# Optimization experiments

Hardware: AMD Instinct MI355X
Metric: run time of the kernel (lower is better)

The kernel has to match this reference:

```python
import jax, jax.numpy as jnp
import numpy as np


def setup_inputs() -> dict:
    key = jax.random.key(0)
    k1, k2 = jax.random.split(key)
    B, Q, LD, D = 64, 32, 4096, 128
    query_embeds = jax.random.normal(k1, (B, Q, D), dtype=jnp.float32)
    doc_embeds = jax.random.normal(k2, (B, LD, D), dtype=jnp.float32)
    return {"query_embeds": query_embeds, "doc_embeds": doc_embeds}


def reference(query_embeds, doc_embeds):
    # ColBERT MaxSim (similarity_metric='maxsim'):
    # torch: (q.unsqueeze(2) * d.unsqueeze(1)).sum(-1).max(dim=-1).values.sum(-1)
    # Efficient equivalent: batched GEMM then max over doc tokens, sum over query tokens.
    # scores: [B, Q, Ld]
    scores = jnp.einsum('bqd,bld->bql', query_embeds, doc_embeds)
    # max over doc tokens (Ld), sum over query tokens (Q) -> [B]
    return jnp.max(scores, axis=-1).sum(axis=-1)
```

## Files before the change

### kernel.cpp

```cpp
#include <hip/hip_runtime.h>
#include <hip/hip_bf16.h>

typedef __attribute__((ext_vector_type(8))) short bf16x8;
typedef __attribute__((ext_vector_type(4))) float f32x4;

static constexpr int Bb = 64;
static constexpr int Qq = 32;
static constexpr int LD = 4096;
static constexpr int Dd = 128;
static constexpr int SPLITS = 16;
static constexpr int CHUNK = LD / SPLITS;
static constexpr int TILE = 32;
static constexpr int ITERS = CHUNK / TILE;
static constexpr int TILE_BYTES = TILE * Dd * 4;
static constexpr int ROW_BYTES = Dd * 4;

__device__ __forceinline__ short f2bf(float f) {
  __hip_bfloat16 h = __float2bfloat16(f);
  return *reinterpret_cast<short*>(&h);
}

__device__ __forceinline__ bf16x8 cvt8(float4 a, float4 b) {
  bf16x8 v;
  v[0] = f2bf(a.x); v[1] = f2bf(a.y); v[2] = f2bf(a.z); v[3] = f2bf(a.w);
  v[4] = f2bf(b.x); v[5] = f2bf(b.y); v[6] = f2bf(b.z); v[7] = f2bf(b.w);
  return v;
}

__device__ __forceinline__ void gload16(const void* g, void* l) {
  __builtin_amdgcn_global_load_lds(
      (const __attribute__((address_space(1))) void*)g,
      (__attribute__((address_space(3))) void*)l, 16, 0, 0);
}

__global__ __launch_bounds__(256, 4) void maxsim_stage1(
    const float* __restrict__ qe, const float* __restrict__ de,
    float* __restrict__ pmax) {
  __shared__ __align__(16) char lds[2][TILE_BYTES];

  const int blk  = blockIdx.x;
  const int b    = blk / SPLITS;
  const int s    = blk % SPLITS;
  const int wave = threadIdx.x >> 6;
  const int lane = threadIdx.x & 63;
  const int lcol = lane & 15;
  const int lgrp = lane >> 4;
  const int mt   = wave >> 1;
  const int half = wave & 1;

  const float* __restrict__ qb = qe + (size_t)b * Qq * Dd;
  const char*  __restrict__ dchunk =
      (const char*)(de + (size_t)b * LD * Dd) + (size_t)s * CHUNK * ROW_BYTES;

  bf16x8 afrag[4];
#pragma unroll
  for (int kb = 0; kb < 4; ++kb) {
    const float* p = qb + (size_t)(mt * 16 + lcol) * Dd + kb * 32 + lgrp * 8;
    afrag[kb] = cvt8(*reinterpret_cast<const float4*>(p),
                     *reinterpret_cast<const float4*>(p + 4));
  }

  auto STAGE = [&](int it, int bufi) {
    const char* itb = dchunk + (size_t)it * TILE_BYTES;
#pragma unroll
    for (int i = 0; i < 4; ++i) {
      unsigned P = (unsigned)(i * 4096 + wave * 1024 + lane * 16);
      unsigned G = P ^ (((P >> 9) & 7u) << 4);
      gload16(itb + G, &lds[bufi][i * 4096 + wave * 1024]);
    }
  };

  float mx[4];
#pragma unroll
  for (int i = 0; i < 4; ++i) mx[i] = -3.4e38f;

  const int row = half * 16 + lcol;
  const unsigned sw = ((unsigned)(lcol & 7)) << 4;

  STAGE(0, 0);
  __syncthreads();

  for (int it = 0; it < ITERS; ++it) {
    const int cur = it & 1;
    if (it + 1 < ITERS) STAGE(it + 1, cur ^ 1);

    const char* base = &lds[cur][row * ROW_BYTES];
    f32x4 acc = {0.f, 0.f, 0.f, 0.f};
#pragma unroll
    for (int kb = 0; kb < 4; ++kb) {
      unsigned o0 = ((unsigned)(kb * 128 + lgrp * 32)) ^ sw;
      unsigned o1 = ((unsigned)(kb * 128 + lgrp * 32 + 16)) ^ sw;
      float4 f0 = *reinterpret_cast<const float4*>(base + o0);
      float4 f1 = *reinterpret_cast<const float4*>(base + o1);
      bf16x8 bf = cvt8(f0, f1);
      acc = __builtin_amdgcn_mfma_f32_16x16x32_bf16(afrag[kb], bf, acc, 0, 0, 0);
    }
#pragma unroll
    for (int i = 0; i < 4; ++i) mx[i] = fmaxf(mx[i], acc[i]);

    __syncthreads();
  }

#pragma unroll
  for (int off = 1; off < 16; off <<= 1)
#pragma unroll
    for (int i = 0; i < 4; ++i) mx[i] = fmaxf(mx[i], __shfl_xor(mx[i], off));

  __shared__ float smax[4][16];
  if (lcol == 0) {
#pragma unroll
    for (int i = 0; i < 4; ++i) smax[wave][lgrp * 4 + i] = mx[i];
  }
  __syncthreads();
  if (threadIdx.x < Qq) {
    const int qi = threadIdx.x;
    const int qmt = qi >> 4, qr = qi & 15;
    float m = fmaxf(smax[qmt * 2 + 0][qr], smax[qmt * 2 + 1][qr]);
    pmax[((size_t)b * SPLITS + s) * Qq + qi] = m;
  }
}

__global__ __launch_bounds__(64) void maxsim_stage2(
    const float* __restrict__ pmax, float* __restrict__ out) {
  const int b = blockIdx.x;
  const int lane = threadIdx.x;
  float v = 0.f;
  if (lane < Qq) {
    float m = -3.4e38f;
#pragma unroll
    for (int s = 0; s < SPLITS; ++s)
      m = fmaxf(m, pmax[((size_t)b * SPLITS + s) * Qq + lane]);
    v = m;
  }
#pragma unroll
  for (int off = 1; off < 64; off <<= 1) v += __shfl_xor(v, off);
  if (lane == 0) out[b] = v;
}

extern "C" void kernel_launch(void* const* d_in, const int* in_sizes, int n_in,
                              void* d_out, int out_size, void* d_ws, size_t ws_size,
                              hipStream_t stream) {
  const float* qe = (const float*)d_in[0];
  const float* de = (const float*)d_in[1];
  float* out  = (float*)d_out;
  float* pmax = (float*)d_ws;

  maxsim_stage1<<<Bb * SPLITS, 256, 0, stream>>>(qe, de, pmax);
  maxsim_stage2<<<Bb, 64, 0, stream>>>(pmax, out);
}
```

Measured before the change: 28.58 us.

## Triple-buffer doc tiles with vmcnt waits instead of full syncthreads

Doc tiles are now streamed through three LDS buffers, prefetching two tiles ahead. The per-iteration __syncthreads is replaced by an explicit s_waitcnt vmcnt plus a raw s_barrier, so more async global-to-LDS loads stay in flight. The min-blocks-per-CU launch-bounds hint is dropped, and the larger LDS footprint lowers possible occupancy. There is also no barrier between one iteration's compute and the next prefetch into the buffer just read, so a fast wave could overwrite a tile a slow wave is still reading.

```diff
diff --git a/kernel.cpp b/kernel.cpp
--- a/kernel.cpp
+++ b/kernel.cpp
@@ -14,6 +14,7 @@
 static constexpr int ITERS = CHUNK / TILE;
 static constexpr int TILE_BYTES = TILE * Dd * 4;
 static constexpr int ROW_BYTES = Dd * 4;
+static constexpr int NBUF = 3;
 
 __device__ __forceinline__ short f2bf(float f) {
   __hip_bfloat16 h = __float2bfloat16(f);
@@ -33,10 +34,12 @@
       (__attribute__((address_space(3))) void*)l, 16, 0, 0);
 }
 
-__global__ __launch_bounds__(256, 4) void maxsim_stage1(
+#define WAIT_VMCNT(n) asm volatile("s_waitcnt vmcnt(" #n ")" ::: "memory")
+
+__global__ __launch_bounds__(256) void maxsim_stage1(
     const float* __restrict__ qe, const float* __restrict__ de,
     float* __restrict__ pmax) {
-  __shared__ __align__(16) char lds[2][TILE_BYTES];
+  __shared__ __align__(16) char lds[NBUF][TILE_BYTES];
 
   const int blk  = blockIdx.x;
   const int b    = blk / SPLITS;
@@ -77,14 +80,8 @@
   const int row = half * 16 + lcol;
   const unsigned sw = ((unsigned)(lcol & 7)) << 4;
 
-  STAGE(0, 0);
-  __syncthreads();
-
-  for (int it = 0; it < ITERS; ++it) {
-    const int cur = it & 1;
-    if (it + 1 < ITERS) STAGE(it + 1, cur ^ 1);
-
-    const char* base = &lds[cur][row * ROW_BYTES];
+  auto COMPUTE = [&](int bufi) {
+    const char* base = &lds[bufi][row * ROW_BYTES];
     f32x4 acc = {0.f, 0.f, 0.f, 0.f};
 #pragma unroll
     for (int kb = 0; kb < 4; ++kb) {
@@ -97,9 +94,31 @@
     }
 #pragma unroll
     for (int i = 0; i < 4; ++i) mx[i] = fmaxf(mx[i], acc[i]);
+  };
 
-    __syncthreads();
+  STAGE(0, 0);
+  STAGE(1, 1);
+
+  int nb = 2;
+  int cb = 0;
+  for (int it = 0; it < ITERS - 2; ++it) {
+    STAGE(it + 2, nb);
+    WAIT_VMCNT(8);
+    __builtin_amdgcn_s_barrier();
+    asm volatile("" ::: "memory");
+    COMPUTE(cb);
+    nb = (nb == 2) ? 0 : nb + 1;
+    cb = (cb == 2) ? 0 : cb + 1;
   }
+  WAIT_VMCNT(4);
+  __builtin_amdgcn_s_barrier();
+  asm volatile("" ::: "memory");
+  COMPUTE(cb);
+  cb = (cb == 2) ? 0 : cb + 1;
+  WAIT_VMCNT(0);
+  __builtin_amdgcn_s_barrier();
+  asm volatile("" ::: "memory");
+  COMPUTE(cb);
 
 #pragma unroll
   for (int off = 1; off < 16; off <<= 1)
```

Result: no change. 29.04 us (+1.6%).

## Replace direct global-to-LDS loads with register-staged two-deep prefetch pipeline

Applied to the files above, without the earlier changes.

Stops using global_load_lds. Each tile is now loaded into registers two iterations ahead, written to LDS, and followed by a single barrier per step. The loop is fully unrolled over double-buffered register sets, and the occupancy hint of 4 blocks per CU is removed from launch bounds. The aim is to keep more global loads in flight and cut per-iteration sync overhead, at the cost of more VGPRs and the LDS write instructions that global_load_lds had avoided.

```diff
diff --git a/kernel.cpp b/kernel.cpp
--- a/kernel.cpp
+++ b/kernel.cpp
@@ -27,13 +27,7 @@
   return v;
 }
 
-__device__ __forceinline__ void gload16(const void* g, void* l) {
-  __builtin_amdgcn_global_load_lds(
-      (const __attribute__((address_space(1))) void*)g,
-      (__attribute__((address_space(3))) void*)l, 16, 0, 0);
-}
-
-__global__ __launch_bounds__(256, 4) void maxsim_stage1(
+__global__ __launch_bounds__(256) void maxsim_stage1(
     const float* __restrict__ qe, const float* __restrict__ de,
     float* __restrict__ pmax) {
   __shared__ __align__(16) char lds[2][TILE_BYTES];
@@ -60,14 +54,24 @@
                      *reinterpret_cast<const float4*>(p + 4));
   }
 
-  auto STAGE = [&](int it, int bufi) {
+  unsigned Poff[4], Goff[4];
+#pragma unroll
+  for (int i = 0; i < 4; ++i) {
+    unsigned P = (unsigned)(i * 4096 + wave * 1024 + lane * 16);
+    Poff[i] = P;
+    Goff[i] = P ^ (((P >> 9) & 7u) << 4);
+  }
+
+  auto LOADR = [&](int it, float4 (&stg)[4]) {
     const char* itb = dchunk + (size_t)it * TILE_BYTES;
 #pragma unroll
-    for (int i = 0; i < 4; ++i) {
-      unsigned P = (unsigned)(i * 4096 + wave * 1024 + lane * 16);
-      unsigned G = P ^ (((P >> 9) & 7u) << 4);
-      gload16(itb + G, &lds[bufi][i * 4096 + wave * 1024]);
-    }
+    for (int i = 0; i < 4; ++i)
+      stg[i] = *reinterpret_cast<const float4*>(itb + Goff[i]);
+  };
+  auto WRITELDS = [&](int bufi, float4 (&stg)[4]) {
+#pragma unroll
+    for (int i = 0; i < 4; ++i)
+      *reinterpret_cast<float4*>(&lds[bufi][Poff[i]]) = stg[i];
   };
 
   float mx[4];
@@ -77,14 +81,8 @@
   const int row = half * 16 + lcol;
   const unsigned sw = ((unsigned)(lcol & 7)) << 4;
 
-  STAGE(0, 0);
-  __syncthreads();
-
-  for (int it = 0; it < ITERS; ++it) {
-    const int cur = it & 1;
-    if (it + 1 < ITERS) STAGE(it + 1, cur ^ 1);
-
-    const char* base = &lds[cur][row * ROW_BYTES];
+  auto COMPUTE = [&](int bufi) {
+    const char* base = &lds[bufi][row * ROW_BYTES];
     f32x4 acc = {0.f, 0.f, 0.f, 0.f};
 #pragma unroll
     for (int kb = 0; kb < 4; ++kb) {
@@ -92,13 +90,29 @@
       unsigned o1 = ((unsigned)(kb * 128 + lgrp * 32 + 16)) ^ sw;
       float4 f0 = *reinterpret_cast<const float4*>(base + o0);
       float4 f1 = *reinterpret_cast<const float4*>(base + o1);
-      bf16x8 bf = cvt8(f0, f1);
-      acc = __builtin_amdgcn_mfma_f32_16x16x32_bf16(afrag[kb], bf, acc, 0, 0, 0);
+      acc = __builtin_amdgcn_mfma_f32_16x16x32_bf16(afrag[kb], cvt8(f0, f1),
+                                                    acc, 0, 0, 0);
     }
 #pragma unroll
     for (int i = 0; i < 4; ++i) mx[i] = fmaxf(mx[i], acc[i]);
+  };
 
-    __syncthreads();
+  auto STEP = [&](int it, int bufi, float4 (&stg)[4]) {
+    WRITELDS(bufi, stg);
+    asm volatile("s_waitcnt lgkmcnt(0)" ::: "memory");
+    __builtin_amdgcn_s_barrier();
+    asm volatile("" ::: "memory");
+    if (it + 2 < ITERS) LOADR(it + 2, stg);
+    COMPUTE(bufi);
+  };
+
+  float4 s0[4], s1[4];
+  LOADR(0, s0);
+  LOADR(1, s1);
+#pragma unroll
+  for (int it = 0; it < ITERS; it += 2) {
+    STEP(it,     0, s0);
+    STEP(it + 1, 1, s1);
   }
 
 #pragma unroll
```

Measured after the change: 30.70 us. 1.07x slower.

## Double split count, halve tile, alternate waves per tile with vmcnt waits

Applied to the files above, without the earlier changes.

Doubles the document-token splits to 32, which doubles the block count, and halves the staged tile to 16 rows. Occupancy is raised to 8 blocks per CU. Each wave pair now owns alternating tiles rather than half of each tile, and the end-of-iteration __syncthreads is replaced by explicit s_waitcnt vmcnt plus a raw s_barrier. The aim is to increase parallelism and shorten per-iteration sync. In exchange, half the waves idle on each tile, and a wave may issue the next async LDS load into a buffer that waves of the other parity are still reading, which is a potential write-after-read race.

```diff
diff --git a/kernel.cpp b/kernel.cpp
--- a/kernel.cpp
+++ b/kernel.cpp
@@ -8,9 +8,9 @@
 static constexpr int Qq = 32;
 static constexpr int LD = 4096;
 static constexpr int Dd = 128;
-static constexpr int SPLITS = 16;
+static constexpr int SPLITS = 32;
 static constexpr int CHUNK = LD / SPLITS;
-static constexpr int TILE = 32;
+static constexpr int TILE = 16;
 static constexpr int ITERS = CHUNK / TILE;
 static constexpr int TILE_BYTES = TILE * Dd * 4;
 static constexpr int ROW_BYTES = Dd * 4;
@@ -33,7 +33,9 @@
       (__attribute__((address_space(3))) void*)l, 16, 0, 0);
 }
 
-__global__ __launch_bounds__(256, 4) void maxsim_stage1(
+#define WAIT_VMCNT(n) asm volatile("s_waitcnt vmcnt(" #n ")" ::: "memory")
+
+__global__ __launch_bounds__(256, 8) void maxsim_stage1(
     const float* __restrict__ qe, const float* __restrict__ de,
     float* __restrict__ pmax) {
   __shared__ __align__(16) char lds[2][TILE_BYTES];
@@ -45,8 +47,8 @@
   const int lane = threadIdx.x & 63;
   const int lcol = lane & 15;
   const int lgrp = lane >> 4;
-  const int mt   = wave >> 1;
-  const int half = wave & 1;
+  const int mt   = wave & 1;
+  const int par  = wave >> 1;
 
   const float* __restrict__ qb = qe + (size_t)b * Qq * Dd;
   const char*  __restrict__ dchunk =
@@ -63,7 +65,7 @@
   auto STAGE = [&](int it, int bufi) {
     const char* itb = dchunk + (size_t)it * TILE_BYTES;
 #pragma unroll
-    for (int i = 0; i < 4; ++i) {
+    for (int i = 0; i < 2; ++i) {
       unsigned P = (unsigned)(i * 4096 + wave * 1024 + lane * 16);
       unsigned G = P ^ (((P >> 9) & 7u) << 4);
       gload16(itb + G, &lds[bufi][i * 4096 + wave * 1024]);
@@ -74,17 +76,10 @@
 #pragma unroll
   for (int i = 0; i < 4; ++i) mx[i] = -3.4e38f;
 
-  const int row = half * 16 + lcol;
   const unsigned sw = ((unsigned)(lcol & 7)) << 4;
 
-  STAGE(0, 0);
-  __syncthreads();
-
-  for (int it = 0; it < ITERS; ++it) {
-    const int cur = it & 1;
-    if (it + 1 < ITERS) STAGE(it + 1, cur ^ 1);
-
-    const char* base = &lds[cur][row * ROW_BYTES];
+  auto COMPUTE = [&](int bufi) {
+    const char* base = &lds[bufi][lcol * ROW_BYTES];
     f32x4 acc = {0.f, 0.f, 0.f, 0.f};
 #pragma unroll
     for (int kb = 0; kb < 4; ++kb) {
@@ -92,13 +87,25 @@
       unsigned o1 = ((unsigned)(kb * 128 + lgrp * 32 + 16)) ^ sw;
       float4 f0 = *reinterpret_cast<const float4*>(base + o0);
       float4 f1 = *reinterpret_cast<const float4*>(base + o1);
-      bf16x8 bf = cvt8(f0, f1);
-      acc = __builtin_amdgcn_mfma_f32_16x16x32_bf16(afrag[kb], bf, acc, 0, 0, 0);
+      acc = __builtin_amdgcn_mfma_f32_16x16x32_bf16(afrag[kb], cvt8(f0, f1),
+                                                    acc, 0, 0, 0);
     }
 #pragma unroll
     for (int i = 0; i < 4; ++i) mx[i] = fmaxf(mx[i], acc[i]);
+  };
 
-    __syncthreads();
+  STAGE(0, 0);
+#pragma unroll
+  for (int it = 0; it < ITERS; ++it) {
+    if (it + 1 < ITERS) {
+      STAGE(it + 1, (it + 1) & 1);
+      WAIT_VMCNT(2);
+    } else {
+      WAIT_VMCNT(0);
+    }
+    __builtin_amdgcn_s_barrier();
+    asm volatile("" ::: "memory");
+    if (par == (it & 1)) COMPUTE(it & 1);
   }
 
 #pragma unroll
@@ -115,7 +122,7 @@
   if (threadIdx.x < Qq) {
     const int qi = threadIdx.x;
     const int qmt = qi >> 4, qr = qi & 15;
-    float m = fmaxf(smax[qmt * 2 + 0][qr], smax[qmt * 2 + 1][qr]);
+    float m = fmaxf(smax[qmt][qr], smax[2 + qmt][qr]);
     pmax[((size_t)b * SPLITS + s) * Qq + qi] = m;
   }
 }
```

After: 29.03 us. Within noise of the previous version (+1.6%).
